# Kernel tuning notes

Measured on AMD Instinct MI355X. Metric: run time of the kernel, lower is better.

Reference implementation:

```python
import jax, jax.numpy as jnp
import numpy as np

B, T, C = 4, 1024, 512
H, HD = 8, 64
NE, K = 8, 2
FF = 4 * C


def setup_inputs() -> dict:
    key = jax.random.key(0)
    ks = jax.random.split(key, 16)
    s = 0.02
    return {
        "x": jax.random.normal(ks[0], (B, T, C), jnp.float32),
        "ln1_g": jnp.ones((C,), jnp.float32),
        "ln1_b": jnp.zeros((C,), jnp.float32),
        "ln2_g": jnp.ones((C,), jnp.float32),
        "ln2_b": jnp.zeros((C,), jnp.float32),
        "Wq": jax.random.normal(ks[1], (H, C, HD), jnp.float32) * s,
        "Wk": jax.random.normal(ks[2], (H, C, HD), jnp.float32) * s,
        "Wv": jax.random.normal(ks[3], (H, C, HD), jnp.float32) * s,
        "Wp": jax.random.normal(ks[4], (H * HD, C), jnp.float32) * s,
        "bp": jnp.zeros((C,), jnp.float32),
        "Wr": jax.random.normal(ks[5], (C, NE), jnp.float32) * s,
        "br": jnp.zeros((NE,), jnp.float32),
        "W1": jax.random.normal(ks[6], (NE, C, FF), jnp.float32) * s,
        "b1": jnp.zeros((NE, FF), jnp.float32),
        "W2": jax.random.normal(ks[7], (NE, FF, C), jnp.float32) * s,
        "b2": jnp.zeros((NE, C), jnp.float32),
    }


def _ln(x, g, b, eps=1e-5):
    mu = jnp.mean(x, axis=-1, keepdims=True)
    var = jnp.var(x, axis=-1, keepdims=True)
    return (x - mu) * jax.lax.rsqrt(var + eps) * g + b


def reference(x, ln1_g, ln1_b, ln2_g, ln2_b, Wq, Wk, Wv, Wp, bp, Wr, br, W1, b1, W2, b2):
    # --- multi-head causal attention (all heads stacked) ---
    h = _ln(x, ln1_g, ln1_b)
    q = jnp.einsum("btc,hcd->bhtd", h, Wq)
    k = jnp.einsum("btc,hcd->bhtd", h, Wk)
    v = jnp.einsum("btc,hcd->bhtd", h, Wv)
    wei = jnp.einsum("bhtd,bhsd->bhts", q, k) / np.sqrt(HD).astype(np.float32)
    causal = jnp.tril(jnp.ones((T, T), bool))
    wei = jnp.where(causal, wei, -jnp.inf)
    wei = jax.nn.softmax(wei, axis=-1)
    attn = jnp.einsum("bhts,bhsd->bhtd", wei, v)  # [B,H,T,HD]
    attn = attn.transpose(0, 2, 1, 3).reshape(B, T, H * HD)
    x2 = x + attn @ Wp + bp

    # --- SparseMoE: dense all-experts compute, masked top-k combine ---
    h2 = _ln(x2, ln2_g, ln2_b)
    scores = h2 @ Wr + br  # [B,T,NE]
    topk_scores, indices = jax.lax.top_k(scores, K)
    # scatter top-k scores into zeros (rest stays 0), then softmax over experts
    mask = jnp.sum(jax.nn.one_hot(indices, NE, dtype=scores.dtype) * topk_scores[..., None], axis=-2)
    router = jax.nn.softmax(mask, axis=-1)  # [B,T,NE]
    hid = jax.nn.relu(jnp.einsum("btc,ecf->btef", h2, W1) + b1)  # [B,T,NE,FF]
    eo = jnp.einsum("btef,efc->btec", hid, W2) + b2  # [B,T,NE,C]
    moe = jnp.einsum("bte,btec->btc", router, eo)
    return x2 + moe
```

## Files before the change

kernel.cpp:

```cpp
#include <hip/hip_runtime.h>


typedef unsigned short u16;
typedef __attribute__((ext_vector_type(8))) short s16x8;
typedef __attribute__((ext_vector_type(4))) float f32x4;

__device__ __forceinline__ u16 f2bf(float f) {
  union { float f; unsigned u; } v; v.f = f;
  unsigned r = v.u + 0x7fffu + ((v.u >> 16) & 1u);
  return (u16)(r >> 16);
}
__device__ __forceinline__ float bf2f(u16 h) {
  union { unsigned u; float f; } v; v.u = ((unsigned)h) << 16;
  return v.f;
}

#define GLDS16(g, s) __builtin_amdgcn_global_load_lds( \
    (const __attribute__((address_space(1))) void*)(g), \
    (__attribute__((address_space(3))) void*)(s), 16, 0, 0)

#define MFMA16(a, b, c) __builtin_amdgcn_mfma_f32_16x16x32_bf16((a), (b), (c), 0, 0, 0)

__global__ __launch_bounds__(256) void transpose_k(
    const float* __restrict__ in, u16* __restrict__ out,
    int R, int C, long long ibs, long long obs, float scale)
{
  __shared__ float tile[32][33];
  in  += (long long)blockIdx.z * ibs;
  out += (long long)blockIdx.z * obs;
  const int c0 = blockIdx.x * 32, r0 = blockIdx.y * 32;
  const int tx = threadIdx.x, ty = threadIdx.y;
  #pragma unroll
  for (int i = 0; i < 4; ++i)
    tile[ty + i*8][tx] = in[(size_t)(r0 + ty + i*8) * C + c0 + tx];
  __syncthreads();
  #pragma unroll
  for (int i = 0; i < 4; ++i)
    out[(size_t)(c0 + ty + i*8) * R + r0 + tx] = f2bf(tile[tx][ty + i*8] * scale);
}

__global__ __launch_bounds__(256) void transqkv_k(
    const float* __restrict__ Wq, const float* __restrict__ Wk,
    const float* __restrict__ Wv, const float* __restrict__ Wp,
    u16* __restrict__ oqkv, u16* __restrict__ owp)
{
  __shared__ float tile[32][33];
  const int z = blockIdx.z;
  const int tx = threadIdx.x, ty = threadIdx.y;
  if (z < 24) {
    const int which = z >> 3, head = z & 7;
    const float* in = (which == 0 ? Wq : (which == 1 ? Wk : Wv)) + (size_t)head * 512 * 64;
    u16* o = oqkv + (size_t)which * 512 * 512 + (size_t)head * 64 * 512;
    const float scale = (which == 0) ? 0.125f : 1.f;
    const int c0 = blockIdx.x * 32, r0 = blockIdx.y * 32;
    #pragma unroll
    for (int i = 0; i < 4; ++i)
      tile[ty + i*8][tx] = in[(size_t)(r0 + ty + i*8) * 64 + c0 + tx];
    __syncthreads();
    #pragma unroll
    for (int i = 0; i < 4; ++i)
      o[(size_t)(c0 + ty + i*8) * 512 + r0 + tx] = f2bf(tile[tx][ty + i*8] * scale);
  } else {
    const int zz = z - 24;
    const int c0 = (zz * 2 + blockIdx.x) * 32;
    const int r0 = blockIdx.y * 32;
    #pragma unroll
    for (int i = 0; i < 4; ++i)
      tile[ty + i*8][tx] = Wp[(size_t)(r0 + ty + i*8) * 512 + c0 + tx];
    __syncthreads();
    #pragma unroll
    for (int i = 0; i < 4; ++i)
      owp[(size_t)(c0 + ty + i*8) * 512 + r0 + tx] = f2bf(tile[tx][ty + i*8]);
  }
}

__global__ __launch_bounds__(256) void vtrans_k(
    const u16* __restrict__ qkv, u16* __restrict__ vt)
{
  __shared__ u16 tile[32][33];
  const int bh = blockIdx.z, b = bh >> 3, h = bh & 7;
  const int t0 = blockIdx.x * 32, d0 = blockIdx.y * 32;
  const int tx = threadIdx.x, ty = threadIdx.y;
  #pragma unroll
  for (int i = 0; i < 4; ++i)
    tile[ty + i*8][tx] = qkv[(size_t)(b*1024 + t0 + ty + i*8) * 1536 + 1024 + h*64 + d0 + tx];
  __syncthreads();
  #pragma unroll
  for (int i = 0; i < 4; ++i)
    vt[(size_t)bh*65536 + (size_t)(d0 + ty + i*8) * 1024 + t0 + tx] = tile[tx][ty + i*8];
}

__global__ __launch_bounds__(256) void ln_k(
    const float* __restrict__ x, const float* __restrict__ g,
    const float* __restrict__ b, u16* __restrict__ o)
{
  const int row = blockIdx.x, t = threadIdx.x;
  const float* xr = x + (size_t)row * 512;
  const float a0 = xr[t], a1 = xr[t + 256];
  float s = a0 + a1, ss = a0*a0 + a1*a1;
  #pragma unroll
  for (int off = 1; off < 64; off <<= 1) {
    s  += __shfl_xor(s, off);
    ss += __shfl_xor(ss, off);
  }
  __shared__ float rs[4], rq[4];
  const int w = t >> 6;
  if ((t & 63) == 0) { rs[w] = s; rq[w] = ss; }
  __syncthreads();
  s  = rs[0] + rs[1] + rs[2] + rs[3];
  ss = rq[0] + rq[1] + rq[2] + rq[3];
  const float mu = s * (1.f/512.f);
  const float var = ss * (1.f/512.f) - mu*mu;
  const float rstd = rsqrtf(var + 1e-5f);
  o[(size_t)row*512 + t]       = f2bf((a0 - mu) * rstd * g[t]     + b[t]);
  o[(size_t)row*512 + t + 256] = f2bf((a1 - mu) * rstd * g[t+256] + b[t+256]);
}

template<int BN, int EPI>
__global__ __launch_bounds__(256) void gemm2p(
    const u16* __restrict__ A, const u16* __restrict__ Bt,
    int M, int N, int K, int lda, int ldb,
    u16* __restrict__ obf, float* __restrict__ oa,
    const float* __restrict__ bias, const float* __restrict__ extra, int e0)
{
  constexpr int NB = BN / 32;
  constexpr int SB = BN / 32;
  __shared__ u16 Asm[2][128*64];
  __shared__ u16 Bsm[2][BN*64];
  const int t = threadIdx.x, l = t & 63;
  const int wid = t >> 6, wr = wid >> 1, wc = wid & 1;
  const int lrow = l & 15, lhi = l >> 4;
  const int m0 = blockIdx.x * 128, n0 = blockIdx.y * BN;

  const f32x4 z4 = {0.f, 0.f, 0.f, 0.f};
  f32x4 acc[4][NB];
  #pragma unroll
  for (int i = 0; i < 4; ++i)
    #pragma unroll
    for (int j = 0; j < NB; ++j) acc[i][j] = z4;

  const int csw = ((t & 7) ^ ((t >> 3) & 7)) * 8;
  const u16* ga = A  + (size_t)(m0 + (t >> 3)) * lda + csw;
  const u16* gb = Bt + (size_t)(n0 + (t >> 3)) * ldb + csw;

#define STG2(buf, k0) do { \
    _Pragma("unroll") \
    for (int i = 0; i < 4; ++i) \
      GLDS16(ga + (size_t)(i*32)*lda + (k0), (char*)Asm[buf] + i*4096 + t*16); \
    _Pragma("unroll") \
    for (int i = 0; i < SB; ++i) \
      GLDS16(gb + (size_t)(i*32)*ldb + (k0), (char*)Bsm[buf] + i*4096 + t*16); \
  } while (0)

#define RD2(Ls, row, kb) (*(const s16x8*)((const char*)(Ls) + (row)*128 + ((kb) ^ (((row)&7)<<4))))

  const int NT = K >> 6;
  STG2(0, 0);
  for (int tt = 0; tt < NT; ++tt) {
    if (tt + 1 < NT) {
      STG2((tt + 1) & 1, (tt + 1) * 64);
      if constexpr (BN == 128)     asm volatile("s_waitcnt vmcnt(8)" ::: "memory");
      else if constexpr (BN == 96) asm volatile("s_waitcnt vmcnt(7)" ::: "memory");
      else                         asm volatile("s_waitcnt vmcnt(6)" ::: "memory");
    } else {
      asm volatile("s_waitcnt vmcnt(0)" ::: "memory");
    }
    __builtin_amdgcn_sched_barrier(0);
    __builtin_amdgcn_s_barrier();
    const u16* As = Asm[tt & 1];
    const u16* Bs = Bsm[tt & 1];
    #pragma unroll
    for (int kh = 0; kh < 2; ++kh) {
      s16x8 af[4], bfr[NB];
      #pragma unroll
      for (int i = 0; i < 4; ++i)
        af[i]  = RD2(As, wr*64 + i*16 + lrow, kh*64 + lhi*16);
      #pragma unroll
      for (int j = 0; j < NB; ++j)
        bfr[j] = RD2(Bs, wc*(BN/2) + j*16 + lrow, kh*64 + lhi*16);
      #pragma unroll
      for (int i = 0; i < 4; ++i)
        #pragma unroll
        for (int j = 0; j < NB; ++j)
          acc[i][j] = MFMA16(af[i], bfr[j], acc[i][j]);
    }
    __builtin_amdgcn_s_barrier();
    __builtin_amdgcn_sched_barrier(0);
  }
#undef STG2
#undef RD2

  #pragma unroll
  for (int i = 0; i < 4; ++i) {
    const int rbase = m0 + wr*64 + i*16 + lhi*4;
    #pragma unroll
    for (int j = 0; j < NB; ++j) {
      const int col = n0 + wc*(BN/2) + j*16 + lrow;
      #pragma unroll
      for (int rr = 0; rr < 4; ++rr) {
        const int row = rbase + rr;
        const float v = acc[i][j][rr];
        if (EPI == 0) {
          obf[(size_t)row*N + col] = f2bf(v);
        } else if (EPI == 1) {
          const float r = extra[(size_t)row*8 + e0 + (col >> 11)];
          obf[(size_t)row*N + col] = f2bf(fmaxf(v + bias[col], 0.f) * r);
        } else {
          oa[(size_t)row*N + col] = v + bias[col] + extra[(size_t)row*N + col];
        }
      }
    }
  }
}

template<int NKT, int EPI>
__global__ __launch_bounds__(512, 2) void gemm8p(
    const u16* __restrict__ A, const u16* __restrict__ Bt,
    int lda, int ldb,
    u16* __restrict__ obf,
    const float* __restrict__ bias, const float* __restrict__ rout)
{
  __shared__ u16 Lds[2][2][256*64];
  const int t = threadIdx.x, l = t & 63;
  const int wid = t >> 6, wm = wid >> 2, wn = wid & 3;
  const int lrow = l & 15, lhi = l >> 4;

  int m0, n0, zz = 0;
  {
    const int bid = blockIdx.x;
    const int r = bid & 7, k = bid >> 3;
    if (EPI == 1) {
      m0 = (k >> 3) * 256; n0 = (r * 8 + (k & 7)) * 256;
    } else if (EPI == 2) {
      n0 = (r * 8 + (k & 7)) * 256; m0 = (k >> 3) * 256;
    } else if (EPI == 4) {
      zz = r*4 + (k & 3);
      const int mn = k >> 2;
      m0 = (mn >> 1) * 256; n0 = (mn & 1) * 256;
    } else {
      zz = r*2 + (k & 1);
      const int mn = k >> 1;
      m0 = (mn >> 1) * 256; n0 = (mn & 1) * 256;
    }
  }
  constexpr int KCH = (EPI == 4) ? 512 : 1024;
  const u16* Ab = A  + (size_t)m0 * lda + ((EPI == 4 || EPI == 5) ? zz * KCH : 0);
  const u16* Bb = Bt + (size_t)n0 * ldb + ((EPI == 4 || EPI == 5) ? zz * KCH : 0);

  const int tr = t >> 3;
  const int sc = ((t & 7) ^ (tr & 7)) * 8;

#define STGU(bf, kt, op_, u4_) do { \
    const u16* s_ = (op_) ? Bb : Ab; \
    const int ld_ = (op_) ? ldb : lda; \
    GLDS16(s_ + (size_t)((u4_)*64 + tr) * ld_ + (size_t)(kt)*64 + sc, \
           (char*)&Lds[bf][op_][0] + (u4_)*8192 + t*16); \
  } while (0)

#define RD(Ls, row, kb) (*(const s16x8*)((const char*)(Ls) + (row)*128 + ((kb) ^ (((row)&7)<<4))))

  f32x4 acc[8][4];
  const f32x4 z4 = {0.f, 0.f, 0.f, 0.f};
  #pragma unroll
  for (int i = 0; i < 8; ++i)
    #pragma unroll
    for (int j = 0; j < 4; ++j) acc[i][j] = z4;

  #pragma unroll
  for (int u = 0; u < 4; ++u) STGU(0, 0, 0, u);
  #pragma unroll
  for (int u = 0; u < 4; ++u) STGU(0, 0, 1, u);
  if (NKT > 1) {
    #pragma unroll
    for (int u = 0; u < 4; ++u) STGU(1, 1, 1, u);
    asm volatile("s_waitcnt vmcnt(4)" ::: "memory");
  } else {
    asm volatile("s_waitcnt vmcnt(0)" ::: "memory");
  }
  __builtin_amdgcn_sched_barrier(0);
  __builtin_amdgcn_s_barrier();

  s16x8 frA[2][4], frB[2][4];
  #pragma unroll 2
  for (int X = 0; X < NKT; ++X) {
    const u16* As = &Lds[X & 1][0][0];
    const u16* Bs = &Lds[X & 1][1][0];
    #pragma unroll
    for (int kk = 0; kk < 2; ++kk) {
      #pragma unroll
      for (int nf = 0; nf < 4; ++nf)
        frB[kk][nf] = RD(Bs, wn*64 + nf*16 + lrow, kk*64 + lhi*16);
      #pragma unroll
      for (int mf = 0; mf < 4; ++mf)
        frA[kk][mf] = RD(As, wm*128 + mf*16 + lrow, kk*64 + lhi*16);
    }
    if (X + 1 < NKT) {
      #pragma unroll
      for (int u = 0; u < 4; ++u) STGU((X + 1) & 1, X + 1, 0, u);
    }
    __builtin_amdgcn_s_barrier();
    asm volatile("s_waitcnt lgkmcnt(0)" ::: "memory");
    __builtin_amdgcn_sched_barrier(0);
    __builtin_amdgcn_s_setprio(1);
    #pragma unroll
    for (int kk = 0; kk < 2; ++kk)
      #pragma unroll
      for (int mf = 0; mf < 4; ++mf)
        #pragma unroll
        for (int nf = 0; nf < 4; ++nf)
          acc[mf][nf] = MFMA16(frA[kk][mf], frB[kk][nf], acc[mf][nf]);
    __builtin_amdgcn_s_setprio(0);
    __builtin_amdgcn_s_barrier();
    #pragma unroll
    for (int kk = 0; kk < 2; ++kk)
      #pragma unroll
      for (int mf = 0; mf < 4; ++mf)
        frA[kk][mf] = RD(As, wm*128 + 64 + mf*16 + lrow, kk*64 + lhi*16);
    if (X + 2 < NKT) {
      #pragma unroll
      for (int u = 0; u < 4; ++u) STGU(X & 1, X + 2, 1, u);
    }
    __builtin_amdgcn_s_barrier();
    asm volatile("s_waitcnt lgkmcnt(0)" ::: "memory");
    __builtin_amdgcn_sched_barrier(0);
    __builtin_amdgcn_s_setprio(1);
    #pragma unroll
    for (int kk = 0; kk < 2; ++kk)
      #pragma unroll
      for (int mf = 0; mf < 4; ++mf)
        #pragma unroll
        for (int nf = 0; nf < 4; ++nf)
          acc[4 + mf][nf] = MFMA16(frA[kk][mf], frB[kk][nf], acc[4 + mf][nf]);
    __builtin_amdgcn_s_setprio(0);
    if (X + 1 < NKT) {
      if (X + 2 < NKT) asm volatile("s_waitcnt vmcnt(4)" ::: "memory");
      else             asm volatile("s_waitcnt vmcnt(0)" ::: "memory");
      __builtin_amdgcn_sched_barrier(0);
    }
    __builtin_amdgcn_s_barrier();
  }
#undef STGU
#undef RD

  constexpr size_t PSTRIDE = (EPI == 4) ? (size_t)1024*512 : (size_t)2048*512;
  u16* outp = (EPI == 4 || EPI == 5) ? obf + (size_t)zz * PSTRIDE : obf;
  #pragma unroll
  for (int mf = 0; mf < 8; ++mf) {
    const int rbase = m0 + wm*128 + mf*16 + lhi*4;
    #pragma unroll
    for (int nf = 0; nf < 4; ++nf) {
      const int col = n0 + wn*64 + nf*16 + lrow;
      #pragma unroll
      for (int rr = 0; rr < 4; ++rr) {
        const int row = rbase + rr;
        float v = acc[mf][nf][rr];
        if (EPI == 1 || EPI == 2) {
          const float r = rout[(size_t)row*8 + (col >> 11)];
          outp[(size_t)row*16384 + col] = f2bf(fmaxf(v + bias[col], 0.f) * r);
        } else {
          outp[(size_t)row*512 + col] = f2bf(v);
        }
      }
    }
  }
}

template<int Z>
__global__ __launch_bounds__(256) void combineZ_k(
    float* __restrict__ outq, const u16* __restrict__ P, size_t pstride,
    const float* __restrict__ routq, const float* __restrict__ b2)
{
  const int row = blockIdx.x, t = threadIdx.x;
  const int c = t * 2;
  float r[8];
  #pragma unroll
  for (int e = 0; e < 8; ++e) r[e] = routq[(size_t)row*8 + e];
  float v0 = outq[(size_t)row*512 + c];
  float v1 = outq[(size_t)row*512 + c + 1];
  #pragma unroll
  for (int z = 0; z < Z; ++z) {
    const unsigned pv = *(const unsigned*)(P + (size_t)z*pstride + (size_t)row*512 + c);
    v0 += bf2f((u16)(pv & 0xffffu));
    v1 += bf2f((u16)(pv >> 16));
  }
  #pragma unroll
  for (int e = 0; e < 8; ++e) {
    v0 += r[e] * b2[(size_t)e*512 + c];
    v1 += r[e] * b2[(size_t)e*512 + c + 1];
  }
  outq[(size_t)row*512 + c]     = v0;
  outq[(size_t)row*512 + c + 1] = v1;
}

__global__ __launch_bounds__(256) void gemm2_k(
    const u16* __restrict__ hid, const u16* __restrict__ w2t,
    u16* __restrict__ P, int e0, int accum)
{
  __shared__ u16 Asm[128*64];
  __shared__ u16 Bsm[64*64];
  const int t = threadIdx.x;
  const int l = t & 63;
  const int wid = t >> 6, wr = wid >> 1, wc = wid & 1;
  const int lrow = l & 15, lhi = l >> 4;
  const int m0 = blockIdx.x * 128, n0 = blockIdx.y * 64, z = blockIdx.z;

  const u16* A  = hid + z * 2048;
  const u16* Bt = w2t + (size_t)(e0 + z) * 512 * 2048;
  u16* Pz = P + (size_t)z * 4096 * 512;

  const f32x4 z4 = {0.f, 0.f, 0.f, 0.f};
  f32x4 acc[4][2];
  #pragma unroll
  for (int i = 0; i < 4; ++i) { acc[i][0] = z4; acc[i][1] = z4; }

  const u16* ga = A  + (size_t)(m0 + (t >> 3)) * 4096 + (t & 7) * 8;
  const u16* gb = Bt + (size_t)(n0 + (t >> 3)) * 2048 + (t & 7) * 8;

  for (int k0 = 0; k0 < 2048; k0 += 64) {
    #pragma unroll
    for (int i = 0; i < 4; ++i)
      GLDS16(ga + (size_t)i*32*4096 + k0, (char*)Asm + i*4096 + t*16);
    #pragma unroll
    for (int i = 0; i < 2; ++i)
      GLDS16(gb + (size_t)i*32*2048 + k0, (char*)Bsm + i*4096 + t*16);
    __syncthreads();
    #pragma unroll
    for (int kh = 0; kh < 2; ++kh) {
      s16x8 af[4], bfr[2];
      #pragma unroll
      for (int i = 0; i < 4; ++i)
        af[i]  = *(const s16x8*)(Asm + (wr*64 + i*16 + lrow)*64 + kh*32 + lhi*8);
      #pragma unroll
      for (int j = 0; j < 2; ++j)
        bfr[j] = *(const s16x8*)(Bsm + (wc*32 + j*16 + lrow)*64 + kh*32 + lhi*8);
      #pragma unroll
      for (int i = 0; i < 4; ++i)
        #pragma unroll
        for (int j = 0; j < 2; ++j)
          acc[i][j] = MFMA16(af[i], bfr[j], acc[i][j]);
    }
    __syncthreads();
  }

  #pragma unroll
  for (int i = 0; i < 4; ++i) {
    const int rbase = m0 + wr*64 + i*16 + lhi*4;
    #pragma unroll
    for (int j = 0; j < 2; ++j) {
      const int col = n0 + wc*32 + j*16 + lrow;
      #pragma unroll
      for (int rr = 0; rr < 4; ++rr) {
        const size_t idx = (size_t)(rbase + rr) * 512 + col;
        const float old = accum ? bf2f(Pz[idx]) : 0.f;
        Pz[idx] = f2bf(old + acc[i][j][rr]);
      }
    }
  }
}

__global__ __launch_bounds__(256) void combineB_k(
    float* __restrict__ out, const u16* __restrict__ P,
    const float* __restrict__ rout, const float* __restrict__ b2)
{
  const int row = blockIdx.x, t = threadIdx.x;
  float r[8];
  #pragma unroll
  for (int e = 0; e < 8; ++e) r[e] = rout[(size_t)row*8 + e];
  #pragma unroll
  for (int cc = 0; cc < 2; ++cc) {
    const int c = t + cc*256;
    const size_t idx = (size_t)row*512 + c;
    float v = out[idx] + bf2f(P[idx]) + bf2f(P[(size_t)4096*512 + idx]);
    #pragma unroll
    for (int e = 0; e < 8; ++e) v += r[e] * b2[(size_t)e*512 + c];
    out[idx] = v;
  }
}

__global__ __launch_bounds__(256) void attn_k(
    const u16* __restrict__ qkv, const u16* __restrict__ vt, u16* __restrict__ o)
{
  const int bid = blockIdx.x;
  const int xcd = bid & 7, rr_ = bid >> 3;
  const int bh = (rr_ >> 3) * 8 + xcd;
  const int qp = rr_ & 7;
  const int b = bh >> 3, h = bh & 7;
  const int t = threadIdx.x, l = t & 63, w = t >> 6;
  const int lrow = l & 15, lhi = l >> 4;

  __shared__ u16 Ksm[2][64*64];
  __shared__ u16 Vsm[2][64*64];
  __shared__ u16 Psm[4][16][72];

  const int trow = t >> 3;
  const int csw = ((t & 7) ^ (trow & 7)) * 8;
  const u16* gk = qkv + (size_t)(b*1024 + trow) * 1536 + 512 + h*64 + csw;
  const u16* gv = vt + (size_t)bh*65536 + (size_t)trow*1024 + csw;
  const f32x4 z4 = {0.f,0.f,0.f,0.f};

#define ASTAGE(buf, s0) do { \
    _Pragma("unroll") \
    for (int i = 0; i < 2; ++i) { \
      GLDS16(gk + (size_t)((s0) + i*32) * 1536, (char*)Ksm[buf] + i*4096 + t*16); \
      GLDS16(gv + (s0) + (size_t)(i*32)*1024,   (char*)Vsm[buf] + i*4096 + t*16); \
    } } while (0)

  for (int pass = 0; pass < 2; ++pass) {
    const int qb = pass ? (15 - qp) : qp;
    const int t0w = qb*64 + w*16;
    const u16* qrow = qkv + (size_t)(b*1024 + t0w + lrow) * 1536 + h*64 + lhi*8;
    s16x8 qf0 = *(const s16x8*)qrow;
    s16x8 qf1 = *(const s16x8*)(qrow + 32);

    float m[4], sl[4];
    f32x4 oacc[4];
    #pragma unroll
    for (int i = 0; i < 4; ++i) { m[i] = -1e30f; sl[i] = 0.f; oacc[i] = z4; }

    const int nt = qb + 1;
    ASTAGE(0, 0);
    for (int kv = 0; kv < nt; ++kv) {
      const int s0 = kv * 64;
      if (kv + 1 < nt) {
        ASTAGE((kv + 1) & 1, s0 + 64);
        asm volatile("s_waitcnt vmcnt(4)" ::: "memory");
      } else {
        asm volatile("s_waitcnt vmcnt(0)" ::: "memory");
      }
      __builtin_amdgcn_s_barrier();
      __builtin_amdgcn_sched_barrier(0);
      const u16* Ks = Ksm[kv & 1];
      const u16* Vs = Vsm[kv & 1];

      f32x4 sacc[4] = {z4, z4, z4, z4};
      #pragma unroll
      for (int n = 0; n < 4; ++n) {
        const int r = n*16 + lrow;
        s16x8 kf0 = *(const s16x8*)((const char*)Ks + r*128 + ((lhi*16) ^ ((r & 7) << 4)));
        s16x8 kf1 = *(const s16x8*)((const char*)Ks + r*128 + ((64 + lhi*16) ^ ((r & 7) << 4)));
        sacc[n] = MFMA16(qf0, kf0, sacc[n]);
        sacc[n] = MFMA16(qf1, kf1, sacc[n]);
      }
      if (s0 + 63 > t0w) {
        #pragma unroll
        for (int n = 0; n < 4; ++n)
          #pragma unroll
          for (int rr = 0; rr < 4; ++rr)
            if (s0 + n*16 + lrow > t0w + lhi*4 + rr) sacc[n][rr] = -1e30f;
      }
      float pm[4];
      #pragma unroll
      for (int rr = 0; rr < 4; ++rr)
        pm[rr] = fmaxf(fmaxf(sacc[0][rr], sacc[1][rr]), fmaxf(sacc[2][rr], sacc[3][rr]));
      #pragma unroll
      for (int rr = 0; rr < 4; ++rr) {
        pm[rr] = fmaxf(pm[rr], __shfl_xor(pm[rr], 1));
        pm[rr] = fmaxf(pm[rr], __shfl_xor(pm[rr], 2));
        pm[rr] = fmaxf(pm[rr], __shfl_xor(pm[rr], 4));
        pm[rr] = fmaxf(pm[rr], __shfl_xor(pm[rr], 8));
      }
      float p[4][4], ps[4], scv[4];
      #pragma unroll
      for (int rr = 0; rr < 4; ++rr) {
        const float mn = fmaxf(m[rr], pm[rr]);
        scv[rr] = __expf(m[rr] - mn);
        m[rr] = mn;
        ps[rr] = 0.f;
        #pragma unroll
        for (int n = 0; n < 4; ++n) {
          p[n][rr] = __expf(sacc[n][rr] - mn);
          ps[rr] += p[n][rr];
        }
      }
      #pragma unroll
      for (int rr = 0; rr < 4; ++rr) {
        ps[rr] += __shfl_xor(ps[rr], 1);
        ps[rr] += __shfl_xor(ps[rr], 2);
        ps[rr] += __shfl_xor(ps[rr], 4);
        ps[rr] += __shfl_xor(ps[rr], 8);
        sl[rr] = sl[rr] * scv[rr] + ps[rr];
      }
      #pragma unroll
      for (int ct = 0; ct < 4; ++ct) {
        f32x4 t4 = oacc[ct];
        #pragma unroll
        for (int rr = 0; rr < 4; ++rr) t4[rr] *= scv[rr];
        oacc[ct] = t4;
      }
      #pragma unroll
      for (int n = 0; n < 4; ++n)
        #pragma unroll
        for (int rr = 0; rr < 4; ++rr)
          Psm[w][lhi*4 + rr][n*16 + lrow] = f2bf(p[n][rr]);
      asm volatile("s_waitcnt lgkmcnt(0)" ::: "memory");
      __builtin_amdgcn_sched_barrier(0);
      s16x8 pa0 = *(const s16x8*)&Psm[w][lrow][lhi*8];
      s16x8 pa1 = *(const s16x8*)&Psm[w][lrow][32 + lhi*8];
      #pragma unroll
      for (int ct = 0; ct < 4; ++ct) {
        const int r = ct*16 + lrow;
        s16x8 vb0 = *(const s16x8*)((const char*)Vs + r*128 + ((lhi*16) ^ ((r & 7) << 4)));
        s16x8 vb1 = *(const s16x8*)((const char*)Vs + r*128 + ((64 + lhi*16) ^ ((r & 7) << 4)));
        oacc[ct] = MFMA16(pa0, vb0, oacc[ct]);
        oacc[ct] = MFMA16(pa1, vb1, oacc[ct]);
      }
      __builtin_amdgcn_s_barrier();
      __builtin_amdgcn_sched_barrier(0);
    }
    #pragma unroll
    for (int ct = 0; ct < 4; ++ct)
      #pragma unroll
      for (int rr = 0; rr < 4; ++rr) {
        const int row = b*1024 + t0w + lhi*4 + rr;
        o[(size_t)row*512 + h*64 + ct*16 + lrow] = f2bf(oacc[ct][rr] / sl[rr]);
      }
  }
#undef ASTAGE
}

__global__ __launch_bounds__(256) void router_k(
    const float* __restrict__ x2, const float* __restrict__ g,
    const float* __restrict__ b, const float* __restrict__ Wr,
    const float* __restrict__ br, float* __restrict__ rt,
    u16* __restrict__ h2o)
{
  const int l = threadIdx.x & 63, w = threadIdx.x >> 6;
  const int tkn = blockIdx.x * 4 + w;
  const float* xr = x2 + (size_t)tkn * 512;
  float v[8];
  float s = 0.f, ss = 0.f;
  #pragma unroll
  for (int i = 0; i < 8; ++i) {
    v[i] = xr[l*8 + i];
    s += v[i]; ss += v[i]*v[i];
  }
  #pragma unroll
  for (int off = 1; off < 64; off <<= 1) {
    s  += __shfl_xor(s, off);
    ss += __shfl_xor(ss, off);
  }
  const float mu = s * (1.f/512.f);
  const float var = ss * (1.f/512.f) - mu*mu;
  const float rstd = rsqrtf(var + 1e-5f);
  float acc[8];
  #pragma unroll
  for (int e = 0; e < 8; ++e) acc[e] = 0.f;
  s16x8 hw;
  #pragma unroll
  for (int i = 0; i < 8; ++i) {
    const int c = l*8 + i;
    const float hv = (v[i] - mu) * rstd * g[c] + b[c];
    hw[i] = (short)f2bf(hv);
    const float* wrow = Wr + (size_t)c * 8;
    #pragma unroll
    for (int e = 0; e < 8; ++e) acc[e] += hv * wrow[e];
  }
  *(s16x8*)(h2o + (size_t)tkn*512 + l*8) = hw;
  #pragma unroll
  for (int e = 0; e < 8; ++e) {
    #pragma unroll
    for (int off = 1; off < 64; off <<= 1) acc[e] += __shfl_xor(acc[e], off);
    acc[e] += br[e];
  }
  int e1 = 0;
  #pragma unroll
  for (int e = 1; e < 8; ++e) if (acc[e] > acc[e1]) e1 = e;
  int e2 = (e1 == 0) ? 1 : 0;
  #pragma unroll
  for (int e = 0; e < 8; ++e) if (e != e1 && acc[e] > acc[e2]) e2 = e;
  const float mx = fmaxf(acc[e1], 0.f);
  float Z = 0.f;
  #pragma unroll
  for (int e = 0; e < 8; ++e) {
    const float mv = (e == e1 || e == e2) ? acc[e] : 0.f;
    Z += __expf(mv - mx);
  }
  if (l < 8) {
    const float mv = (l == e1 || l == e2) ? acc[l] : 0.f;
    rt[(size_t)tkn * 8 + l] = __expf(mv - mx) / Z;
  }
}

extern "C" void kernel_launch(void* const* d_in, const int* in_sizes, int n_in,
                              void* d_out, int out_size, void* d_ws, size_t ws_size,
                              hipStream_t stream) {
  const float* x    = (const float*)d_in[0];
  const float* ln1g = (const float*)d_in[1];
  const float* ln1b = (const float*)d_in[2];
  const float* ln2g = (const float*)d_in[3];
  const float* ln2b = (const float*)d_in[4];
  const float* Wq   = (const float*)d_in[5];
  const float* Wk   = (const float*)d_in[6];
  const float* Wv   = (const float*)d_in[7];
  const float* Wp   = (const float*)d_in[8];
  const float* bp   = (const float*)d_in[9];
  const float* Wr   = (const float*)d_in[10];
  const float* br   = (const float*)d_in[11];
  const float* W1   = (const float*)d_in[12];
  const float* b1   = (const float*)d_in[13];
  const float* W2   = (const float*)d_in[14];
  const float* b2   = (const float*)d_in[15];
  float* out = (float*)d_out;

  const int pathH = (ws_size >= (size_t)138543104) ? 1 : 0;
  const int pathN = (ws_size >= (size_t)104988672) ? 1 : 0;

  char* ws = (char*)d_ws;
  size_t off = 0;
  auto alloc = [&](size_t bytes) -> char* {
    char* p = ws + off;
    off += (bytes + 255) & ~(size_t)255;
    return p;
  };
  u16* w1_t = (u16*)alloc((size_t)8*2048*512*2);
  u16* w2f  = (u16*)alloc((size_t)8*512*2048*2);
  u16* h2b  = (u16*)alloc((size_t)4096*512*2);
  float* rout = (float*)alloc((size_t)4096*8*4);
  u16* hidq = (u16*)alloc(pathH ? (size_t)2048*16384*2 : (size_t)4096*4096*2);
  u16* Ppl  = (u16*)alloc(pathH ? (size_t)16*2048*512*2
                                : (pathN ? (size_t)32*1024*512*2 : (size_t)2*4096*512*2));
  u16* wqkv_t = (u16*)hidq;
  u16* wp_t   = (u16*)((char*)hidq + 1572864);
  u16* hb     = (u16*)((char*)hidq + 2097152);
  u16* attnb  = (u16*)((char*)hidq + 6291456);
  u16* qkvb   = (u16*)((char*)hidq + 10485760);
  u16* vtb    = (u16*)((char*)hidq + 23068672);

  const dim3 tb(32, 8);
  transqkv_k<<<dim3(2,16,32), tb, 0, stream>>>(Wq, Wk, Wv, Wp, wqkv_t, wp_t);
  transpose_k<<<dim3(64,16,8), tb, 0, stream>>>(W1, w1_t, 512, 2048, (long long)512*2048, (long long)2048*512, 1.f);
  if (pathN)
    transpose_k<<<dim3(16,512,1), tb, 0, stream>>>(W2, w2f, 16384, 512, 0, 0, 1.f);
  else
    transpose_k<<<dim3(16,64,8), tb, 0, stream>>>(W2, w2f, 2048, 512, (long long)2048*512, (long long)512*2048, 1.f);

  ln_k<<<4096, 256, 0, stream>>>(x, ln1g, ln1b, hb);
  gemm2p<96,0><<<dim3(32,16), 256, 0, stream>>>(hb, wqkv_t, 4096, 1536, 512, 512, 512,
                                                qkvb, nullptr, nullptr, nullptr, 0);
  vtrans_k<<<dim3(32,2,32), tb, 0, stream>>>(qkvb, vtb);
  attn_k<<<256, 256, 0, stream>>>(qkvb, vtb, attnb);
  gemm2p<64,2><<<dim3(32,8), 256, 0, stream>>>(attnb, wp_t, 4096, 512, 512, 512, 512,
                                               nullptr, out, bp, x, 0);
  router_k<<<1024, 256, 0, stream>>>(out, ln2g, ln2b, Wr, br, rout, h2b);

  if (pathH) {
    for (int h = 0; h < 2; ++h) {
      gemm8p<8,2><<<512, 512, 0, stream>>>(h2b + (size_t)h*2048*512, w1_t, 512, 512,
                                           hidq, b1, rout + (size_t)h*16384);
      gemm8p<16,5><<<256, 512, 0, stream>>>(hidq, w2f, 16384, 16384,
                                            Ppl, nullptr, nullptr);
      combineZ_k<16><<<2048, 256, 0, stream>>>(out + (size_t)h*2048*512, Ppl,
                                               (size_t)2048*512,
                                               rout + (size_t)h*16384, b2);
    }
  } else if (pathN) {
    for (int q = 0; q < 4; ++q) {
      gemm8p<8,1><<<256, 512, 0, stream>>>(h2b + (size_t)q*1024*512, w1_t, 512, 512,
                                           hidq, b1, rout + (size_t)q*8192);
      gemm8p<8,4><<<256, 512, 0, stream>>>(hidq, w2f, 16384, 16384,
                                           Ppl, nullptr, nullptr);
      combineZ_k<32><<<1024, 256, 0, stream>>>(out + (size_t)q*1024*512, Ppl,
                                               (size_t)1024*512,
                                               rout + (size_t)q*8192, b2);
    }
  } else {
    for (int p = 0; p < 4; ++p) {
      const int e0 = 2*p;
      gemm2p<128,1><<<dim3(32,32), 256, 0, stream>>>(h2b, w1_t + (size_t)e0*2048*512,
                                                     4096, 4096, 512, 512, 512,
                                                     hidq, nullptr, b1 + (size_t)e0*2048, rout, e0);
      gemm2_k<<<dim3(32,8,2), 256, 0, stream>>>(hidq, w2f, Ppl, e0, p > 0 ? 1 : 0);
    }
    combineB_k<<<4096, 256, 0, stream>>>(out, Ppl, rout, b2);
  }
}
```

Measured before the change: 274.6 us.

## Widen attention KV tiles to 128 and fuse W1/W2 weight transposes

The flash-attention kernel now processes 128 keys per iteration instead of 64. This halves the number of loop trips, barriers and softmax rescale steps per query block, at the cost of double the LDS for K, V and P tiles and more registers. A separate change merges the W1 and W2 fp32-to-bf16 transposes into one launch when pathN is active, saving a kernel launch. A catch is that 64-row query blocks at even indices now compute a partly masked 128-key tile, which adds some wasted MFMA work on the diagonal.

```diff
diff --git a/kernel.cpp b/kernel.cpp
--- a/kernel.cpp
+++ b/kernel.cpp
@@ -37,6 +37,38 @@
   #pragma unroll
   for (int i = 0; i < 4; ++i)
     out[(size_t)(c0 + ty + i*8) * R + r0 + tx] = f2bf(tile[tx][ty + i*8] * scale);
+}
+
+__global__ __launch_bounds__(256) void transW_k(
+    const float* __restrict__ W1, const float* __restrict__ W2,
+    u16* __restrict__ w1t, u16* __restrict__ w2f)
+{
+  __shared__ float tile[32][33];
+  const int z = blockIdx.z;
+  const int tx = threadIdx.x, ty = threadIdx.y;
+  if (z < 8) {
+    const float* in = W1 + (size_t)z * 512 * 2048;
+    u16* out = w1t + (size_t)z * 2048 * 512;
+    const int c0 = blockIdx.x * 32, r0 = blockIdx.y * 32;
+    #pragma unroll
+    for (int i = 0; i < 4; ++i)
+      tile[ty + i*8][tx] = in[(size_t)(r0 + ty + i*8) * 2048 + c0 + tx];
+    __syncthreads();
+    #pragma unroll
+    for (int i = 0; i < 4; ++i)
+      out[(size_t)(c0 + ty + i*8) * 512 + r0 + tx] = f2bf(tile[tx][ty + i*8]);
+  } else {
+    const int e = z - 8;
+    const float* in = W2 + (size_t)e * 2048 * 512;
+    const int r0 = blockIdx.x * 32, c0 = blockIdx.y * 32;
+    #pragma unroll
+    for (int i = 0; i < 4; ++i)
+      tile[ty + i*8][tx] = in[(size_t)(r0 + ty + i*8) * 512 + c0 + tx];
+    __syncthreads();
+    #pragma unroll
+    for (int i = 0; i < 4; ++i)
+      w2f[(size_t)(c0 + ty + i*8) * 16384 + e*2048 + r0 + tx] = f2bf(tile[tx][ty + i*8]);
+  }
 }
 
 __global__ __launch_bounds__(256) void transqkv_k(
@@ -488,22 +520,26 @@
   const int t = threadIdx.x, l = t & 63, w = t >> 6;
   const int lrow = l & 15, lhi = l >> 4;
 
-  __shared__ u16 Ksm[2][64*64];
-  __shared__ u16 Vsm[2][64*64];
-  __shared__ u16 Psm[4][16][72];
+  __shared__ u16 Ksm[2][128*64];
+  __shared__ u16 Vsm[2][64*128];
+  __shared__ u16 Psm[4][16][136];
 
   const int trow = t >> 3;
   const int csw = ((t & 7) ^ (trow & 7)) * 8;
+  const int vrow = t >> 4;
+  const int vsw = ((t & 15) ^ (vrow & 7)) * 8;
   const u16* gk = qkv + (size_t)(b*1024 + trow) * 1536 + 512 + h*64 + csw;
-  const u16* gv = vt + (size_t)bh*65536 + (size_t)trow*1024 + csw;
+  const u16* gv = vt + (size_t)bh*65536 + (size_t)vrow*1024 + vsw;
   const f32x4 z4 = {0.f,0.f,0.f,0.f};
 
 #define ASTAGE(buf, s0) do { \
     _Pragma("unroll") \
-    for (int i = 0; i < 2; ++i) { \
+    for (int i = 0; i < 4; ++i) \
       GLDS16(gk + (size_t)((s0) + i*32) * 1536, (char*)Ksm[buf] + i*4096 + t*16); \
-      GLDS16(gv + (s0) + (size_t)(i*32)*1024,   (char*)Vsm[buf] + i*4096 + t*16); \
-    } } while (0)
+    _Pragma("unroll") \
+    for (int i = 0; i < 4; ++i) \
+      GLDS16(gv + (s0) + (size_t)(i*16)*1024,   (char*)Vsm[buf] + i*4096 + t*16); \
+  } while (0)
 
   for (int pass = 0; pass < 2; ++pass) {
     const int qb = pass ? (15 - qp) : qp;
@@ -517,13 +553,13 @@
     #pragma unroll
     for (int i = 0; i < 4; ++i) { m[i] = -1e30f; sl[i] = 0.f; oacc[i] = z4; }
 
-    const int nt = qb + 1;
+    const int nt = (qb >> 1) + 1;
     ASTAGE(0, 0);
     for (int kv = 0; kv < nt; ++kv) {
-      const int s0 = kv * 64;
+      const int s0 = kv * 128;
       if (kv + 1 < nt) {
-        ASTAGE((kv + 1) & 1, s0 + 64);
-        asm volatile("s_waitcnt vmcnt(4)" ::: "memory");
+        ASTAGE((kv + 1) & 1, s0 + 128);
+        asm volatile("s_waitcnt vmcnt(8)" ::: "memory");
       } else {
         asm volatile("s_waitcnt vmcnt(0)" ::: "memory");
       }
@@ -532,26 +568,31 @@
       const u16* Ks = Ksm[kv & 1];
       const u16* Vs = Vsm[kv & 1];
 
-      f32x4 sacc[4] = {z4, z4, z4, z4};
-      #pragma unroll
-      for (int n = 0; n < 4; ++n) {
+      f32x4 sacc[8];
+      #pragma unroll
+      for (int n = 0; n < 8; ++n) sacc[n] = z4;
+      #pragma unroll
+      for (int n = 0; n < 8; ++n) {
         const int r = n*16 + lrow;
         s16x8 kf0 = *(const s16x8*)((const char*)Ks + r*128 + ((lhi*16) ^ ((r & 7) << 4)));
         s16x8 kf1 = *(const s16x8*)((const char*)Ks + r*128 + ((64 + lhi*16) ^ ((r & 7) << 4)));
         sacc[n] = MFMA16(qf0, kf0, sacc[n]);
         sacc[n] = MFMA16(qf1, kf1, sacc[n]);
       }
-      if (s0 + 63 > t0w) {
+      if (s0 + 127 > t0w) {
         #pragma unroll
-        for (int n = 0; n < 4; ++n)
+        for (int n = 0; n < 8; ++n)
           #pragma unroll
           for (int rr = 0; rr < 4; ++rr)
             if (s0 + n*16 + lrow > t0w + lhi*4 + rr) sacc[n][rr] = -1e30f;
       }
       float pm[4];
       #pragma unroll
-      for (int rr = 0; rr < 4; ++rr)
-        pm[rr] = fmaxf(fmaxf(sacc[0][rr], sacc[1][rr]), fmaxf(sacc[2][rr], sacc[3][rr]));
+      for (int rr = 0; rr < 4; ++rr) {
+        float a = fmaxf(fmaxf(sacc[0][rr], sacc[1][rr]), fmaxf(sacc[2][rr], sacc[3][rr]));
+        float bmx = fmaxf(fmaxf(sacc[4][rr], sacc[5][rr]), fmaxf(sacc[6][rr], sacc[7][rr]));
+        pm[rr] = fmaxf(a, bmx);
+      }
       #pragma unroll
       for (int rr = 0; rr < 4; ++rr) {
         pm[rr] = fmaxf(pm[rr], __shfl_xor(pm[rr], 1));
@@ -559,7 +600,7 @@
         pm[rr] = fmaxf(pm[rr], __shfl_xor(pm[rr], 4));
         pm[rr] = fmaxf(pm[rr], __shfl_xor(pm[rr], 8));
       }
-      float p[4][4], ps[4], scv[4];
+      float p[8][4], ps[4], scv[4];
       #pragma unroll
       for (int rr = 0; rr < 4; ++rr) {
         const float mn = fmaxf(m[rr], pm[rr]);
@@ -567,7 +608,7 @@
         m[rr] = mn;
         ps[rr] = 0.f;
         #pragma unroll
-        for (int n = 0; n < 4; ++n) {
+        for (int n = 0; n < 8; ++n) {
           p[n][rr] = __expf(sacc[n][rr] - mn);
           ps[rr] += p[n][rr];
         }
@@ -588,21 +629,24 @@
         oacc[ct] = t4;
       }
       #pragma unroll
-      for (int n = 0; n < 4; ++n)
+      for (int n = 0; n < 8; ++n)
         #pragma unroll
         for (int rr = 0; rr < 4; ++rr)
           Psm[w][lhi*4 + rr][n*16 + lrow] = f2bf(p[n][rr]);
       asm volatile("s_waitcnt lgkmcnt(0)" ::: "memory");
       __builtin_amdgcn_sched_barrier(0);
-      s16x8 pa0 = *(const s16x8*)&Psm[w][lrow][lhi*8];
-      s16x8 pa1 = *(const s16x8*)&Psm[w][lrow][32 + lhi*8];
+      s16x8 pa[4];
+      #pragma unroll
+      for (int s = 0; s < 4; ++s)
+        pa[s] = *(const s16x8*)&Psm[w][lrow][s*32 + lhi*8];
       #pragma unroll
       for (int ct = 0; ct < 4; ++ct) {
         const int r = ct*16 + lrow;
-        s16x8 vb0 = *(const s16x8*)((const char*)Vs + r*128 + ((lhi*16) ^ ((r & 7) << 4)));
-        s16x8 vb1 = *(const s16x8*)((const char*)Vs + r*128 + ((64 + lhi*16) ^ ((r & 7) << 4)));
-        oacc[ct] = MFMA16(pa0, vb0, oacc[ct]);
-        oacc[ct] = MFMA16(pa1, vb1, oacc[ct]);
+        #pragma unroll
+        for (int s = 0; s < 4; ++s) {
+          s16x8 vb = *(const s16x8*)((const char*)Vs + r*256 + ((s*64 + lhi*16) ^ ((r & 7) << 4)));
+          oacc[ct] = MFMA16(pa[s], vb, oacc[ct]);
+        }
       }
       __builtin_amdgcn_s_barrier();
       __builtin_amdgcn_sched_barrier(0);
@@ -728,11 +772,14 @@
 
   const dim3 tb(32, 8);
   transqkv_k<<<dim3(2,16,32), tb, 0, stream>>>(Wq, Wk, Wv, Wp, wqkv_t, wp_t);
-  transpose_k<<<dim3(64,16,8), tb, 0, stream>>>(W1, w1_t, 512, 2048, (long long)512*2048, (long long)2048*512, 1.f);
-  if (pathN)
-    transpose_k<<<dim3(16,512,1), tb, 0, stream>>>(W2, w2f, 16384, 512, 0, 0, 1.f);
-  else
-    transpose_k<<<dim3(16,64,8), tb, 0, stream>>>(W2, w2f, 2048, 512, (long long)2048*512, (long long)512*2048, 1.f);
+  if (pathN) {
+    transW_k<<<dim3(64,16,16), tb, 0, stream>>>(W1, W2, w1_t, w2f);
+  } else {
+    transpose_k<<<dim3(64,16,8), tb, 0, stream>>>(W1, w1_t, 512, 2048,
+        (long long)512*2048, (long long)2048*512, 1.f);
+    transpose_k<<<dim3(16,64,8), tb, 0, stream>>>(W2, w2f, 2048, 512,
+        (long long)2048*512, (long long)512*2048, 1.f);
+  }
 
   ln_k<<<4096, 256, 0, stream>>>(x, ln1g, ln1b, hb);
   gemm2p<96,0><<<dim3(32,16), 256, 0, stream>>>(hb, wqkv_t, 4096, 1536, 512, 512, 512,
```

New measurement: 268.0 us, median of 2. -2.4%, faster.
